# Kernel tuning notes

Hardware: AMD Instinct MI355X
Metric: run time of the kernel (lower is better)

## Reference

```python
import jax, jax.numpy as jnp
import numpy as np

NUM_HEADS = 16


def setup_inputs() -> dict:
    key = jax.random.key(0)
    ks = jax.random.split(key, 5)
    B, S, E = 4, 2048, 1024
    scale = 1.0 / np.sqrt(E)
    return {
        "query": jax.random.normal(ks[0], (B, S, E), dtype=jnp.float32),
        "w_in": jax.random.normal(ks[1], (3 * E, E), dtype=jnp.float32) * scale,
        "b_in": jax.random.normal(ks[2], (3 * E,), dtype=jnp.float32) * 0.02,
        "w_out": jax.random.normal(ks[3], (E, E), dtype=jnp.float32) * scale,
        "b_out": jax.random.normal(ks[4], (E,), dtype=jnp.float32) * 0.02,
    }


def reference(query, w_in, b_in, w_out, b_out):
    B, S, E = query.shape
    H = NUM_HEADS
    D = E // H
    # fused QKV projection: [B,S,3E]
    qkv = jnp.einsum('bse,fe->bsf', query, w_in) + b_in
    q, k, v = jnp.split(qkv, 3, axis=-1)
    # [B,H,S,D]
    q = q.reshape(B, S, H, D).transpose(0, 2, 1, 3)
    k = k.reshape(B, S, H, D).transpose(0, 2, 1, 3)
    v = v.reshape(B, S, H, D).transpose(0, 2, 1, 3)
    # scaled dot-product attention with causal mask (is_causal=True, dropout=0)
    scores = jnp.einsum('bhqd,bhkd->bhqk', q, k) * (1.0 / np.sqrt(D))
    causal = jnp.tril(jnp.ones((S, S), dtype=bool))
    scores = jnp.where(causal, scores, jnp.finfo(scores.dtype).min)
    probs = jax.nn.softmax(scores, axis=-1)
    attn = jnp.einsum('bhqk,bhkd->bhqd', probs, v)
    attn = attn.transpose(0, 2, 1, 3).reshape(B, S, E)
    return jnp.einsum('bse,fe->bsf', attn, w_out) + b_out
```

## Files before the change

### kernel.cpp

```cpp
#include <hip/hip_runtime.h>

typedef __bf16 bf16;
typedef __bf16 bf16x4 __attribute__((ext_vector_type(4)));
typedef __bf16 bf16x8 __attribute__((ext_vector_type(8)));
typedef float  f32x4  __attribute__((ext_vector_type(4)));
typedef short  short4v __attribute__((ext_vector_type(4)));

#define GLOAD_LDS16(g, l) __builtin_amdgcn_global_load_lds( \
    (const __attribute__((address_space(1))) void*)(g),     \
    (__attribute__((address_space(3))) void*)(l), 16, 0, 0)

__device__ __forceinline__ float exp2_hw(float x) { return __builtin_amdgcn_exp2f(x); }

#if __has_builtin(__builtin_amdgcn_mfma_f32_16x16x16bf16_1k)
__device__ __forceinline__ f32x4 mfma16(bf16x4 a, bf16x4 b, f32x4 c) {
    return __builtin_amdgcn_mfma_f32_16x16x16bf16_1k(
        __builtin_bit_cast(short4v, a), __builtin_bit_cast(short4v, b), c, 0, 0, 0);
}
#elif __has_builtin(__builtin_amdgcn_mfma_f32_16x16x16_bf16)
__device__ __forceinline__ f32x4 mfma16(bf16x4 a, bf16x4 b, f32x4 c) {
    return __builtin_amdgcn_mfma_f32_16x16x16_bf16(a, b, c, 0, 0, 0);
}
#else
__device__ __forceinline__ f32x4 mfma16(bf16x4 a, bf16x4 b, f32x4 c) {
    asm volatile("v_mfma_f32_16x16x16_bf16 %0, %1, %2, %0"
                 : "+v"(c) : "v"(a), "v"(b));
    return c;
}
#endif

__global__ __launch_bounds__(256) void f32_to_bf16(
    const float* __restrict__ in, bf16* __restrict__ out, int n4)
{
    int i = blockIdx.x * blockDim.x + threadIdx.x;
    const int stride = gridDim.x * blockDim.x;
    for (; i < n4; i += stride) {
        const float4 v = *(const float4*)(in + (size_t)i * 4);
        bf16x4 o = { (bf16)v.x, (bf16)v.y, (bf16)v.z, (bf16)v.w };
        *(bf16x4*)(out + (size_t)i * 4) = o;
    }
}

__global__ __launch_bounds__(256) void conv_rest(
    const float* __restrict__ w_in_f, const float* __restrict__ b_in_f,
    const float* __restrict__ w_out_f, const float* __restrict__ b_out_f,
    bf16* __restrict__ w_in, bf16* __restrict__ b_in,
    bf16* __restrict__ w_out, bf16* __restrict__ b_out)
{
    constexpr int N1 = 786432, N2 = N1 + 768, N3 = N2 + 262144, N4 = N3 + 256;
    int i = blockIdx.x * blockDim.x + threadIdx.x;
    const int stride = gridDim.x * blockDim.x;
    for (; i < N4; i += stride) {
        const float* src; bf16* dst; int off;
        if (i < N1)      { src = w_in_f;  dst = w_in;  off = i; }
        else if (i < N2) { src = b_in_f;  dst = b_in;  off = i - N1; }
        else if (i < N3) { src = w_out_f; dst = w_out; off = i - N2; }
        else             { src = b_out_f; dst = b_out; off = i - N3; }
        const float4 v = *(const float4*)(src + (size_t)off * 4);
        bf16x4 o = { (bf16)v.x, (bf16)v.y, (bf16)v.z, (bf16)v.w };
        *(bf16x4*)(dst + (size_t)off * 4) = o;
    }
}

__device__ __forceinline__ void gemm_mainloop_128(
    const bf16* __restrict__ A, const bf16* __restrict__ B, int K,
    int bm, int bn, bf16* As, bf16* Bs, f32x4 (&acc)[4][4])
{
    const int tid  = threadIdx.x;
    const int lane = tid & 63, fr = lane & 15, fq = lane >> 4;
    const int wave = tid >> 6;
    const int wr   = (wave >> 1) * 64, wc = (wave & 1) * 64;
    const int srow = tid >> 3, sj = tid & 7;
    const int sjs  = (sj ^ (srow & 7)) * 8;
    const int xo0  = (fq ^ (fr & 7)) * 8;
    const int xo1  = ((4 + fq) ^ (fr & 7)) * 8;

    const bf16* Ag = A + (size_t)(bm * 128 + srow) * K + sjs;
    const bf16* Bg = B + (size_t)(bn * 128 + srow) * K + sjs;
    bf16* Asw = As + srow * 64 + sj * 8;
    bf16* Bsw = Bs + srow * 64 + sj * 8;

    for (int k0 = 0; k0 < K; k0 += 64) {
        __syncthreads();
#pragma unroll
        for (int it = 0; it < 4; ++it)
            GLOAD_LDS16(Ag + k0 + (size_t)it * 32 * K, Asw + it * 32 * 64);
#pragma unroll
        for (int it = 0; it < 4; ++it)
            GLOAD_LDS16(Bg + k0 + (size_t)it * 32 * K, Bsw + it * 32 * 64);
        asm volatile("s_waitcnt vmcnt(0)" ::: "memory");
        __syncthreads();

#pragma unroll
        for (int ks = 0; ks < 2; ++ks) {
            const int xo = ks ? xo1 : xo0;
            bf16x8 a[4], b[4];
#pragma unroll
            for (int m = 0; m < 4; ++m)
                a[m] = *(const bf16x8*)&As[(wr + m * 16 + fr) * 64 + xo];
#pragma unroll
            for (int n = 0; n < 4; ++n)
                b[n] = *(const bf16x8*)&Bs[(wc + n * 16 + fr) * 64 + xo];
#pragma unroll
            for (int m = 0; m < 4; ++m)
#pragma unroll
                for (int n = 0; n < 4; ++n)
                    acc[m][n] = __builtin_amdgcn_mfma_f32_16x16x32_bf16(a[m], b[n], acc[m][n], 0, 0, 0);
        }
    }
}

__global__ __launch_bounds__(256) void gemm_qkv(
    const bf16* __restrict__ A, const bf16* __restrict__ B,
    const bf16* __restrict__ bias,
    bf16* __restrict__ qb_, bf16* __restrict__ kb_, bf16* __restrict__ vt_)
{
    constexpr int K = 1024, NTN = 24;
    constexpr float QSCALE = 0.18033688011112042f;
    __shared__ bf16 As[128 * 64];
    __shared__ bf16 Bs[128 * 64];
    const int bm = blockIdx.x / NTN, bn = blockIdx.x % NTN;

    f32x4 acc[4][4] = {};
    gemm_mainloop_128(A, B, K, bm, bn, As, Bs, acc);

    const int tid = threadIdx.x, lane = tid & 63;
    const int fr = lane & 15, fq = lane >> 4;
    const int wave = tid >> 6;
    const int wr = (wave >> 1) * 64, wc = (wave & 1) * 64;

    const int colbase = bn * 128 + wc;
    const int part = colbase >> 10;

#pragma unroll
    for (int n = 0; n < 4; ++n) {
        const int col = colbase + n * 16 + fr;
        const float bv = (float)bias[col];
        const int cl = col & 1023, h = cl >> 6, d = cl & 63;
#pragma unroll
        for (int m = 0; m < 4; ++m) {
            const int row0 = bm * 128 + wr + m * 16 + fq * 4;
            const int bb = row0 >> 11, s0 = row0 & 2047;
            const int bh = bb * 16 + h;
            if (part == 0) {
#pragma unroll
                for (int j = 0; j < 4; ++j)
                    qb_[((size_t)bh * 2048 + s0 + j) * 64 + d] = (bf16)((acc[m][n][j] + bv) * QSCALE);
            } else if (part == 1) {
#pragma unroll
                for (int j = 0; j < 4; ++j)
                    kb_[((size_t)bh * 2048 + s0 + j) * 64 + d] = (bf16)(acc[m][n][j] + bv);
            } else {
                bf16x4 o;
#pragma unroll
                for (int j = 0; j < 4; ++j) o[j] = (bf16)(acc[m][n][j] + bv);
                *(bf16x4*)&vt_[((size_t)bh * 64 + d) * 2048 + s0] = o;
            }
        }
    }
}

__global__ __launch_bounds__(256) void gemm_out(
    const bf16* __restrict__ A, const bf16* __restrict__ B,
    const bf16* __restrict__ bias, float* __restrict__ C)
{
    constexpr int K = 1024, N = 1024, NTN = 8;
    __shared__ bf16 As[128 * 64];
    __shared__ bf16 Bs[128 * 64];
    const int bm = blockIdx.x / NTN, bn = blockIdx.x % NTN;

    f32x4 acc[4][4] = {};
    gemm_mainloop_128(A, B, K, bm, bn, As, Bs, acc);

    const int tid = threadIdx.x, lane = tid & 63;
    const int fr = lane & 15, fq = lane >> 4;
    const int wave = tid >> 6;
    const int wr = (wave >> 1) * 64, wc = (wave & 1) * 64;

#pragma unroll
    for (int n = 0; n < 4; ++n) {
        const int col = bn * 128 + wc + n * 16 + fr;
        const float bv = (float)bias[col];
#pragma unroll
        for (int m = 0; m < 4; ++m) {
            const int row0 = bm * 128 + wr + m * 16 + fq * 4;
#pragma unroll
            for (int j = 0; j < 4; ++j)
                C[(size_t)(row0 + j) * N + col] = acc[m][n][j] + bv;
        }
    }
}

__global__ __launch_bounds__(512, 4) void attn5(
    const bf16* __restrict__ qb_, const bf16* __restrict__ kb_,
    const bf16* __restrict__ vt_, bf16* __restrict__ ctx)
{
    constexpr int S = 2048, EO = 1024;
    constexpr float NEG = -3.0e38f;
    __shared__ bf16 Ks[2][64 * 64];
    __shared__ bf16 Vs[2][64 * 64];

    const int idx = blockIdx.x;
    const int orig = (idx & 7) * 128 + (idx >> 3);
    const int bh = orig >> 4;
    const int qb = 15 - (orig & 15);
    const int bb = bh >> 4, h = bh & 15;

    const int tid = threadIdx.x, lane = tid & 63, wave = tid >> 6;
    const int fr = lane & 15, fq = lane >> 4;

    const bf16* kh = kb_ + (size_t)bh * S * 64;
    const bf16* vh = vt_ + (size_t)bh * 64 * S;
    const bf16* qh = qb_ + (size_t)bh * S * 64;

    const int q0 = qb * 128 + wave * 16;

    bf16x8 qf0, qf1;
    {
        const bf16* qr = qh + (size_t)(q0 + fr) * 64;
        qf0 = *(const bf16x8*)(qr + fq * 8);
        qf1 = *(const bf16x8*)(qr + 32 + fq * 8);
    }

    const int xo0 = (fq ^ (fr & 7)) * 8;
    const int xo1 = ((4 + fq) ^ (fr & 7)) * 8;

    int krb[4], vslot[4], vrow[4];
#pragma unroll
    for (int n = 0; n < 4; ++n) {
        krb[n]   = (n * 16 + fr) * 64;
        vslot[n] = ((n * 2 + (fq >> 1)) ^ (fr & 7)) * 8 + (fq & 1) * 4;
        vrow[n]  = (n * 16 + fr) * 64;
    }

    const int r0 = tid >> 3, j0 = tid & 7;
    const int js = (j0 ^ (r0 & 7)) * 8;

#define STAGE(buf, kt)                                                        \
    do {                                                                      \
        GLOAD_LDS16(kh + (size_t)((kt) * 64 + r0) * 64 + js,                  \
                    &Ks[buf][(r0 * 8 + j0) * 8]);                             \
        GLOAD_LDS16(vh + (size_t)r0 * S + (kt) * 64 + js,                     \
                    &Vs[buf][(r0 * 8 + j0) * 8]);                             \
    } while (0)

    const bf16 one = (bf16)1.0f;
    const bf16x4 ones = { one, one, one, one };

    f32x4 acc[4] = {};
    f32x4 acc1 = {};

    const int ktend = 2 * qb + 1;

    STAGE(0, 0);
    asm volatile("s_waitcnt vmcnt(0)" ::: "memory");
    __syncthreads();

    int cur = 0;
    for (int kt = 0; kt <= ktend; ++kt) {
        if (kt < ktend) STAGE(cur ^ 1, kt + 1);

        const int nmax = (q0 + 15 - kt * 64) >> 4;
        if (nmax >= 0) {
            f32x4 s[4];
            __builtin_amdgcn_s_setprio(1);
#pragma unroll
            for (int n = 0; n < 4; ++n) {
                if (n > nmax) continue;
                s[n] = f32x4{};
                bf16x8 k0v = *(const bf16x8*)&Ks[cur][krb[n] + xo0];
                bf16x8 k1v = *(const bf16x8*)&Ks[cur][krb[n] + xo1];
                s[n] = __builtin_amdgcn_mfma_f32_16x16x32_bf16(k0v, qf0, s[n], 0, 0, 0);
                s[n] = __builtin_amdgcn_mfma_f32_16x16x32_bf16(k1v, qf1, s[n], 0, 0, 0);
            }
            __builtin_amdgcn_s_setprio(0);

            if (nmax <= 3) {
                const int qrel = q0 - kt * 64 + fr;
#pragma unroll
                for (int n = 0; n < 4; ++n) {
                    if (n > nmax) continue;
#pragma unroll
                    for (int j = 0; j < 4; ++j)
                        if (n * 16 + fq * 4 + j > qrel) s[n][j] = NEG;
                }
            }

            bf16x4 pb[4];
#pragma unroll
            for (int n = 0; n < 4; ++n) {
                if (n > nmax) continue;
                pb[n][0] = (bf16)exp2_hw(s[n][0]);
                pb[n][1] = (bf16)exp2_hw(s[n][1]);
                pb[n][2] = (bf16)exp2_hw(s[n][2]);
                pb[n][3] = (bf16)exp2_hw(s[n][3]);
                acc1 = mfma16(pb[n], ones, acc1);
            }

            __builtin_amdgcn_s_setprio(1);
#pragma unroll
            for (int n = 0; n < 4; ++n) {
                if (n > nmax) continue;
#pragma unroll
                for (int n2 = 0; n2 < 4; ++n2) {
                    bf16x4 vf = *(const bf16x4*)&Vs[cur][vrow[n2] + vslot[n]];
                    acc[n2] = mfma16(pb[n], vf, acc[n2]);
                }
            }
            __builtin_amdgcn_s_setprio(0);
        }

        asm volatile("s_waitcnt vmcnt(0)" ::: "memory");
        __syncthreads();
        cur ^= 1;
    }
#undef STAGE

    float linv[4];
#pragma unroll
    for (int j = 0; j < 4; ++j) linv[j] = __builtin_amdgcn_rcpf(acc1[j]);

#pragma unroll
    for (int n2 = 0; n2 < 4; ++n2)
#pragma unroll
        for (int j = 0; j < 4; ++j) {
            int qr_ = q0 + fq * 4 + j;
            ctx[((size_t)bb * S + qr_) * EO + h * 64 + n2 * 16 + fr] = (bf16)(acc[n2][j] * linv[j]);
        }
}

extern "C" void kernel_launch(void* const* d_in, const int* in_sizes, int n_in,
                              void* d_out, int out_size, void* d_ws, size_t ws_size,
                              hipStream_t stream)
{
    constexpr int B = 4, S = 2048, E = 1024;
    constexpr int M = B * S;
    constexpr size_t N_Q  = (size_t)B * S * E;
    constexpr size_t N_WI = (size_t)3 * E * E;
    constexpr size_t N_BI = 3 * E;
    constexpr size_t N_WO = (size_t)E * E;

    const float* query_f = (const float*)d_in[0];
    const float* w_in_f  = (const float*)d_in[1];
    const float* b_in_f  = (const float*)d_in[2];
    const float* w_out_f = (const float*)d_in[3];
    const float* b_out_f = (const float*)d_in[4];
    float* out = (float*)d_out;

    bf16* q_buf = (bf16*)d_ws;
    bf16* k_buf = q_buf + N_Q;
    bf16* vT    = k_buf + N_Q;
    bf16* ctx   = vT + N_Q;
    bf16* query = ctx + N_Q;
    bf16* w_in  = query + N_Q;
    bf16* b_in  = w_in + N_WI;
    bf16* w_out = b_in + N_BI;
    bf16* b_out = w_out + N_WO;

    f32_to_bf16<<<2048, 256, 0, stream>>>(query_f, query, (int)(N_Q / 4));
    conv_rest<<<1024, 256, 0, stream>>>(w_in_f, b_in_f, w_out_f, b_out_f,
                                        w_in, b_in, w_out, b_out);

    gemm_qkv<<<dim3((M / 128) * (3 * E / 128)), 256, 0, stream>>>(
        query, w_in, b_in, q_buf, k_buf, vT);

    attn5<<<dim3(1024), 512, 0, stream>>>(q_buf, k_buf, vT, ctx);

    gemm_out<<<dim3((M / 128) * (E / 128)), 256, 0, stream>>>(
        ctx, w_out, b_out, out);
}
```

Baseline: 191.9 us.

## Process two 16-row query tiles per wave in attention with 256-thread blocks

The attention kernel now uses 4 waves per block instead of 8, and each wave handles 32 query rows as two 16-row tiles. Each K/V fragment read from LDS is reused across both tiles, and each thread stages two rows of K and V per iteration. This halves the LDS fragment reads per query row and the number of waves per block. The cost is more registers per wave, fewer waves to hide latency, and causal masking work handled separately for each tile.

```diff
diff --git a/kernel.cpp b/kernel.cpp
--- a/kernel.cpp
+++ b/kernel.cpp
@@ -191,7 +191,7 @@
     }
 }
 
-__global__ __launch_bounds__(512, 4) void attn5(
+__global__ __launch_bounds__(256, 4) void attn6(
     const bf16* __restrict__ qb_, const bf16* __restrict__ kb_,
     const bf16* __restrict__ vt_, bf16* __restrict__ ctx)
 {
@@ -213,13 +213,16 @@
     const bf16* vh = vt_ + (size_t)bh * 64 * S;
     const bf16* qh = qb_ + (size_t)bh * S * 64;
 
-    const int q0 = qb * 128 + wave * 16;
-
-    bf16x8 qf0, qf1;
+    const int q0 = qb * 128 + wave * 32;
+
+    bf16x8 qfA0, qfA1, qfB0, qfB1;
     {
-        const bf16* qr = qh + (size_t)(q0 + fr) * 64;
-        qf0 = *(const bf16x8*)(qr + fq * 8);
-        qf1 = *(const bf16x8*)(qr + 32 + fq * 8);
+        const bf16* qrA = qh + (size_t)(q0 + fr) * 64;
+        qfA0 = *(const bf16x8*)(qrA + fq * 8);
+        qfA1 = *(const bf16x8*)(qrA + 32 + fq * 8);
+        const bf16* qrB = qh + (size_t)(q0 + 16 + fr) * 64;
+        qfB0 = *(const bf16x8*)(qrB + fq * 8);
+        qfB1 = *(const bf16x8*)(qrB + 32 + fq * 8);
     }
 
     const int xo0 = (fq ^ (fr & 7)) * 8;
@@ -240,15 +243,19 @@
     do {                                                                      \
         GLOAD_LDS16(kh + (size_t)((kt) * 64 + r0) * 64 + js,                  \
                     &Ks[buf][(r0 * 8 + j0) * 8]);                             \
+        GLOAD_LDS16(kh + (size_t)((kt) * 64 + r0 + 32) * 64 + js,             \
+                    &Ks[buf][((r0 + 32) * 8 + j0) * 8]);                      \
         GLOAD_LDS16(vh + (size_t)r0 * S + (kt) * 64 + js,                     \
                     &Vs[buf][(r0 * 8 + j0) * 8]);                             \
+        GLOAD_LDS16(vh + (size_t)(r0 + 32) * S + (kt) * 64 + js,              \
+                    &Vs[buf][((r0 + 32) * 8 + j0) * 8]);                      \
     } while (0)
 
     const bf16 one = (bf16)1.0f;
     const bf16x4 ones = { one, one, one, one };
 
-    f32x4 acc[4] = {};
-    f32x4 acc1 = {};
+    f32x4 accA[4] = {}, accB[4] = {};
+    f32x4 acc1A = {}, acc1B = {};
 
     const int ktend = 2 * qb + 1;
 
@@ -260,51 +267,60 @@
     for (int kt = 0; kt <= ktend; ++kt) {
         if (kt < ktend) STAGE(cur ^ 1, kt + 1);
 
-        const int nmax = (q0 + 15 - kt * 64) >> 4;
-        if (nmax >= 0) {
-            f32x4 s[4];
+        const int base = q0 - kt * 64;
+        const int nmaxA = (base + 15) >> 4;
+        const int nmaxB = (base + 31) >> 4;
+        if (nmaxB >= 0) {
+            bf16x4 pbA[4], pbB[4];
             __builtin_amdgcn_s_setprio(1);
 #pragma unroll
             for (int n = 0; n < 4; ++n) {
-                if (n > nmax) continue;
-                s[n] = f32x4{};
+                if (n > nmaxB) continue;
                 bf16x8 k0v = *(const bf16x8*)&Ks[cur][krb[n] + xo0];
                 bf16x8 k1v = *(const bf16x8*)&Ks[cur][krb[n] + xo1];
-                s[n] = __builtin_amdgcn_mfma_f32_16x16x32_bf16(k0v, qf0, s[n], 0, 0, 0);
-                s[n] = __builtin_amdgcn_mfma_f32_16x16x32_bf16(k1v, qf1, s[n], 0, 0, 0);
-            }
-            __builtin_amdgcn_s_setprio(0);
-
-            if (nmax <= 3) {
-                const int qrel = q0 - kt * 64 + fr;
-#pragma unroll
-                for (int n = 0; n < 4; ++n) {
-                    if (n > nmax) continue;
-#pragma unroll
-                    for (int j = 0; j < 4; ++j)
-                        if (n * 16 + fq * 4 + j > qrel) s[n][j] = NEG;
+                {
+                    f32x4 s = {};
+                    s = __builtin_amdgcn_mfma_f32_16x16x32_bf16(k0v, qfB0, s, 0, 0, 0);
+                    s = __builtin_amdgcn_mfma_f32_16x16x32_bf16(k1v, qfB1, s, 0, 0, 0);
+                    if (nmaxB <= 3) {
+                        const int qrel = base + 16 + fr;
+#pragma unroll
+                        for (int j = 0; j < 4; ++j)
+                            if (n * 16 + fq * 4 + j > qrel) s[j] = NEG;
+                    }
+                    pbB[n][0] = (bf16)exp2_hw(s[0]);
+                    pbB[n][1] = (bf16)exp2_hw(s[1]);
+                    pbB[n][2] = (bf16)exp2_hw(s[2]);
+                    pbB[n][3] = (bf16)exp2_hw(s[3]);
+                    acc1B = mfma16(pbB[n], ones, acc1B);
+                }
+                if (n <= nmaxA) {
+                    f32x4 s = {};
+                    s = __builtin_amdgcn_mfma_f32_16x16x32_bf16(k0v, qfA0, s, 0, 0, 0);
+                    s = __builtin_amdgcn_mfma_f32_16x16x32_bf16(k1v, qfA1, s, 0, 0, 0);
+                    if (nmaxA <= 3) {
+                        const int qrel = base + fr;
+#pragma unroll
+                        for (int j = 0; j < 4; ++j)
+                            if (n * 16 + fq * 4 + j > qrel) s[j] = NEG;
+                    }
+                    pbA[n][0] = (bf16)exp2_hw(s[0]);
+                    pbA[n][1] = (bf16)exp2_hw(s[1]);
+                    pbA[n][2] = (bf16)exp2_hw(s[2]);
+                    pbA[n][3] = (bf16)exp2_hw(s[3]);
+                    acc1A = mfma16(pbA[n], ones, acc1A);
                 }
             }
 
-            bf16x4 pb[4];
 #pragma unroll
             for (int n = 0; n < 4; ++n) {
-                if (n > nmax) continue;
-                pb[n][0] = (bf16)exp2_hw(s[n][0]);
-                pb[n][1] = (bf16)exp2_hw(s[n][1]);
-                pb[n][2] = (bf16)exp2_hw(s[n][2]);
-                pb[n][3] = (bf16)exp2_hw(s[n][3]);
-                acc1 = mfma16(pb[n], ones, acc1);
-            }
-
-            __builtin_amdgcn_s_setprio(1);
-#pragma unroll
-            for (int n = 0; n < 4; ++n) {
-                if (n > nmax) continue;
+                if (n > nmaxB) continue;
 #pragma unroll
                 for (int n2 = 0; n2 < 4; ++n2) {
                     bf16x4 vf = *(const bf16x4*)&Vs[cur][vrow[n2] + vslot[n]];
-                    acc[n2] = mfma16(pb[n], vf, acc[n2]);
+                    accB[n2] = mfma16(pbB[n], vf, accB[n2]);
+                    if (n <= nmaxA)
+                        accA[n2] = mfma16(pbA[n], vf, accA[n2]);
                 }
             }
             __builtin_amdgcn_s_setprio(0);
@@ -316,16 +332,20 @@
     }
 #undef STAGE
 
-    float linv[4];
-#pragma unroll
-    for (int j = 0; j < 4; ++j) linv[j] = __builtin_amdgcn_rcpf(acc1[j]);
-
+    float linvA[4], linvB[4];
+#pragma unroll
+    for (int j = 0; j < 4; ++j) {
+        linvA[j] = __builtin_amdgcn_rcpf(acc1A[j]);
+        linvB[j] = __builtin_amdgcn_rcpf(acc1B[j]);
+    }
 #pragma unroll
     for (int n2 = 0; n2 < 4; ++n2)
 #pragma unroll
         for (int j = 0; j < 4; ++j) {
-            int qr_ = q0 + fq * 4 + j;
-            ctx[((size_t)bb * S + qr_) * EO + h * 64 + n2 * 16 + fr] = (bf16)(acc[n2][j] * linv[j]);
+            const int qA = q0 + fq * 4 + j;
+            ctx[((size_t)bb * S + qA) * EO + h * 64 + n2 * 16 + fr] = (bf16)(accA[n2][j] * linvA[j]);
+            const int qB = q0 + 16 + fq * 4 + j;
+            ctx[((size_t)bb * S + qB) * EO + h * 64 + n2 * 16 + fr] = (bf16)(accB[n2][j] * linvB[j]);
         }
 }
 
@@ -364,7 +384,7 @@
     gemm_qkv<<<dim3((M / 128) * (3 * E / 128)), 256, 0, stream>>>(
         query, w_in, b_in, q_buf, k_buf, vT);
 
-    attn5<<<dim3(1024), 512, 0, stream>>>(q_buf, k_buf, vT, ctx);
+    attn6<<<dim3(1024), 256, 0, stream>>>(q_buf, k_buf, vT, ctx);
 
     gemm_out<<<dim3((M / 128) * (E / 128)), 256, 0, stream>>>(
         ctx, w_out, b_out, out);
```

Result: slower. 471.0 us (+145.4%).
